# Performance work log

Hardware: AMD Instinct MI355X
Metric: run time of the kernel (lower is better)

Reference implementation:

```python
import jax, jax.numpy as jnp
from jax import lax
import numpy as np

B, DIM, NH, H, W = 4, 256, 8, 32, 32
HEAD_DIM = DIM // NH          # 32
KEY_DIM = HEAD_DIM // 2       # attn_ratio = 0.5 -> 16
QKV_OUT = DIM + 2 * NH * KEY_DIM  # 512
SCALE = KEY_DIM ** -0.5


def setup_inputs() -> dict:
    key = jax.random.key(0)
    ks = jax.random.split(key, 11)
    w = lambda k, shape, s=0.05: jax.random.normal(k, shape, jnp.float32) * s
    return {
        "x": jax.random.normal(ks[0], (B, DIM, H, W), jnp.float32),
        "qkv_w": w(ks[1], (QKV_OUT, DIM)),
        "qkv_b": w(ks[2], (QKV_OUT,)),
        "proj_w": w(ks[3], (DIM, DIM)),
        "proj_b": w(ks[4], (DIM,)),
        "pe_w": w(ks[5], (DIM, 1, 3, 3)),
        "pe_b": w(ks[6], (DIM,)),
        "g1_w": w(ks[7], (DIM // 2, DIM)),
        "g1_b": w(ks[8], (DIM // 2,)),
        "g2_w": w(ks[9], (1, DIM // 2)),
        "g2_b": w(ks[10], (1,)),
    }


def conv1x1(x, w, b):
    # fused Conv2d(1x1, bias=False)+BN -> pointwise matmul + bias
    return jnp.einsum('bchw,oc->bohw', x, w) + b[None, :, None, None]


def reference(x, qkv_w, qkv_b, proj_w, proj_b, pe_w, pe_b, g1_w, g1_b, g2_w, g2_b):
    Bx, C, Hh, Ww = x.shape
    N = Hh * Ww
    qkv = conv1x1(x, qkv_w, qkv_b).reshape(Bx, NH, 2 * KEY_DIM + HEAD_DIM, N)
    q = qkv[:, :, :KEY_DIM]                   # [B, nh, key_dim, N]
    k = qkv[:, :, KEY_DIM:2 * KEY_DIM]        # [B, nh, key_dim, N]
    v = qkv[:, :, 2 * KEY_DIM:]               # [B, nh, head_dim, N]

    # attn = q^T @ k * scale  -> [B, nh, N, N]
    attn = jnp.einsum('bhdn,bhdm->bhnm', q, k) * SCALE

    # learned gate -> scalar dynamic k = floor(N * mean(sigmoid(...)))
    g = jax.nn.sigmoid(conv1x1(jax.nn.relu(conv1x1(x, g1_w, g1_b)), g2_w, g2_b))
    dyn_k = jnp.floor(N * jnp.mean(g)).astype(jnp.int32)

    # rank-based top-k mask (jit-friendly equivalent of topk+scatter):
    # keep entries whose descending rank along the last dim is < dyn_k
    order = jnp.argsort(-attn, axis=-1)       # positions sorted by score desc
    ranks = jnp.argsort(order, axis=-1)       # rank of each position
    attn = jnp.where(ranks < dyn_k, attn, -jnp.inf)
    attn = jax.nn.softmax(attn, axis=-1)

    out = jnp.einsum('bhdn,bhmn->bhdm', v, attn).reshape(Bx, C, Hh, Ww)

    # depthwise 3x3 positional-encoding conv on v reshaped to the image grid
    v_img = v.reshape(Bx, C, Hh, Ww)
    pe = lax.conv_general_dilated(
        v_img, pe_w, window_strides=(1, 1), padding=((1, 1), (1, 1)),
        dimension_numbers=('NCHW', 'OIHW', 'NCHW'), feature_group_count=C,
    ) + pe_b[None, :, None, None]

    return conv1x1(out + pe, proj_w, proj_b)
```

## Files before the change

kernel.cpp:

```cpp
#include <hip/hip_runtime.h>
#include <math.h>

#define NTOK 1024
#define CAP 64

#define LDS_FENCE() asm volatile("s_waitcnt lgkmcnt(0)" ::: "memory")

typedef __bf16 bf16x8 __attribute__((ext_vector_type(8)));
typedef unsigned short u16x8 __attribute__((ext_vector_type(8)));
typedef unsigned short u16x4 __attribute__((ext_vector_type(4)));
typedef float f32x4 __attribute__((ext_vector_type(4)));

__device__ __forceinline__ unsigned short f2bf(float f) {
  unsigned int u = __float_as_uint(f);
  return (unsigned short)((u + 0x7fffu + ((u >> 16) & 1u)) >> 16);
}


template<int OC, int OCB, int P, bool RELU, bool VCAST>
__device__ __forceinline__ void conv_body(const float* __restrict__ in,
    const float* __restrict__ w, const float* __restrict__ bias, float* __restrict__ out,
    unsigned short* __restrict__ vbf, int bid, int tid) {
  constexpr int PB = NTOK / (256 * P);
  const int pb = bid % PB; bid /= PB;
  const int ocb = bid % (OC / OCB); const int b = bid / (OC / OCB);
  const int p0 = pb * 256 * P + tid * P;
  const float* inb = in + (size_t)b * 256 * NTOK + p0;
  const float* wrow = w + (size_t)ocb * OCB * 256;

  float acc[OCB][P];
  #pragma unroll
  for (int j = 0; j < OCB; j++)
    #pragma unroll
    for (int i = 0; i < P; i++) acc[j][i] = 0.f;

  #pragma unroll 2
  for (int c0 = 0; c0 < 256; c0 += 4) {
    float4 wl[OCB];
    #pragma unroll
    for (int j = 0; j < OCB; j++) wl[j] = *(const float4*)&wrow[j * 256 + c0];
    #pragma unroll
    for (int cc = 0; cc < 4; cc++) {
      float xr[P];
      if constexpr (P == 4) {
        float4 t = *(const float4*)&inb[(size_t)(c0 + cc) * NTOK];
        xr[0] = t.x; xr[1] = t.y; xr[2] = t.z; xr[3] = t.w;
      } else if constexpr (P == 2) {
        float2 t = *(const float2*)&inb[(size_t)(c0 + cc) * NTOK];
        xr[0] = t.x; xr[1] = t.y;
      } else {
        xr[0] = inb[(size_t)(c0 + cc) * NTOK];
      }
      #pragma unroll
      for (int j = 0; j < OCB; j++) {
        const float wjc = ((const float*)&wl[j])[cc];
        #pragma unroll
        for (int i = 0; i < P; i++) acc[j][i] = fmaf(wjc, xr[i], acc[j][i]);
      }
    }
  }
  #pragma unroll
  for (int j = 0; j < OCB; j++) {
    const int oc = ocb * OCB + j;
    const float bv = bias[oc];
    float r[P];
    #pragma unroll
    for (int i = 0; i < P; i++) {
      float v = acc[j][i] + bv;
      if (RELU) v = fmaxf(v, 0.f);
      r[i] = v;
    }
    float* op = out + ((size_t)b * OC + oc) * NTOK + p0;
    if constexpr (P == 4) *(float4*)op = make_float4(r[0], r[1], r[2], r[3]);
    else if constexpr (P == 2) *(float2*)op = make_float2(r[0], r[1]);
    else *op = r[0];
    if constexpr (VCAST) {
      if ((oc & 63) >= 32) {
        const int c = (oc >> 6) * 32 + (oc & 63) - 32;
        unsigned short* vp = vbf + ((size_t)b * 256 + c) * NTOK + p0;
        #pragma unroll
        for (int i = 0; i < P; i++) vp[i] = f2bf(r[i]);
      }
    }
  }
}

template<int OC, int OCB, int P, bool RELU, bool VCAST>
__global__ __launch_bounds__(256) void conv1x1_kernel(const float* __restrict__ in,
    const float* __restrict__ w, const float* __restrict__ bias, float* __restrict__ out,
    unsigned short* __restrict__ vbf) {
  conv_body<OC, OCB, P, RELU, VCAST>(in, w, bias, out, vbf, blockIdx.x, threadIdx.x);
}

__global__ __launch_bounds__(256) void qkv_gate1_kernel(const float* __restrict__ x,
    const float* __restrict__ qkv_w, const float* __restrict__ qkv_b, float* __restrict__ qkvb,
    unsigned short* __restrict__ vbf,
    const float* __restrict__ g1_w, const float* __restrict__ g1_b, float* __restrict__ gx) {
  const int bid = blockIdx.x;
  if (bid < 512)
    conv_body<512, 8, 2, false, true>(x, qkv_w, qkv_b, qkvb, vbf, bid, threadIdx.x);
  else
    conv_body<128, 8, 2, true, false>(x, g1_w, g1_b, gx, nullptr, bid - 512, threadIdx.x);
}

__global__ __launch_bounds__(256) void gate2_kernel(const float* __restrict__ gx,
    const float* __restrict__ g2_w, const float* __restrict__ g2_b, float* __restrict__ gvals) {
  const int tid = threadIdx.x;
  const int p_l = tid & 15, jg = tid >> 4;
  const int gp = blockIdx.x * 16 + p_l;
  const int b = gp >> 10, p = gp & 1023;
  float s = 0.f;
  const float* gb = gx + ((size_t)b * 128 + jg * 8) * NTOK + p;
  #pragma unroll
  for (int jj = 0; jj < 8; jj++) s = fmaf(g2_w[jg * 8 + jj], gb[(size_t)jj * NTOK], s);
  __shared__ float red[16][17];
  red[jg][p_l] = s;
  __syncthreads();
  if (tid < 16) {
    float a = g2_b[0];
    #pragma unroll
    for (int g = 0; g < 16; g++) a += red[g][tid];
    gvals[blockIdx.x * 16 + tid] = 1.f / (1.f + expf(-a));
  }
}

__global__ void dynk_kernel(const float* __restrict__ gvals, int* __restrict__ dynk) {
  const int t = threadIdx.x;
  double s = 0.0;
  #pragma unroll
  for (int i = 0; i < 16; i++) s += (double)gvals[t + 256 * i];
  __shared__ double red[256];
  red[t] = s;
  __syncthreads();
  for (int st = 128; st > 0; st >>= 1) {
    if (t < st) red[t] += red[t + st];
    __syncthreads();
  }
  if (t == 0) {
    int k = (int)floor(1024.0 * (red[0] / 4096.0));
    *dynk = k < 1 ? 1 : (k > NTOK ? NTOK : k);
  }
}

__global__ __launch_bounds__(512) void attn_kernel(const float* __restrict__ qkv,
    const unsigned short* __restrict__ vbf,
    const int* __restrict__ dynk_p, float* __restrict__ out_attn) {
  const int tid = threadIdx.x;
  const int lane = tid & 63, wv = tid >> 6;
  int bid = blockIdx.x;
  const int mb = bid & 127; bid >>= 7;
  const int h = bid & 7; const int b = bid >> 3;
  const int dyn_k = *dynk_p;

  const float* base = qkv + (size_t)(b * 512 + h * 64) * NTOK;

  __shared__ union RowU { float f[1028]; unsigned short pa[1032]; } rows[8];
  __shared__ float invs[8];
  __shared__ union UU {
    struct {
      int hist[8][64];
      int cnt[8];
      float Bv[8]; int Bn[8];
      struct { float v; int n; } cand[8][CAP];
    } sel;
    float pvred[2][4][8][17];
  } u;

  {
    const float2* k2 = (const float2*)(base + 16 * NTOK);
    const float* qb = base + mb * 8;
    float a0[8], a1[8];
    #pragma unroll
    for (int r = 0; r < 8; r++) { a0[r] = 0.f; a1[r] = 0.f; }
    #pragma unroll
    for (int d = 0; d < 16; d++) {
      float2 kk = k2[d * 512 + tid];
      #pragma unroll
      for (int r = 0; r < 8; r++) {
        const float qv = qb[(size_t)d * NTOK + r];
        a0[r] = fmaf(qv, kk.x, a0[r]);
        a1[r] = fmaf(qv, kk.y, a1[r]);
      }
    }
    #pragma unroll
    for (int r = 0; r < 8; r++)
      ((float2*)rows[r].f)[tid] = make_float2(a0[r] * 0.25f, a1[r] * 0.25f);
  }
  __syncthreads();

  {
    const int r = wv;
    float* smrow = rows[r].f;
    float v[16];
    {
      float4 f0 = ((const float4*)smrow)[lane];
      float4 f1 = ((const float4*)smrow)[64 + lane];
      float4 f2 = ((const float4*)smrow)[128 + lane];
      float4 f3 = ((const float4*)smrow)[192 + lane];
      v[0]=f0.x; v[1]=f0.y; v[2]=f0.z; v[3]=f0.w;
      v[4]=f1.x; v[5]=f1.y; v[6]=f1.z; v[7]=f1.w;
      v[8]=f2.x; v[9]=f2.y; v[10]=f2.z; v[11]=f2.w;
      v[12]=f3.x; v[13]=f3.y; v[14]=f3.z; v[15]=f3.w;
    }
    float mn = v[0], mx = v[0];
    #pragma unroll
    for (int i = 1; i < 16; i++) { mn = fminf(mn, v[i]); mx = fmaxf(mx, v[i]); }
    #pragma unroll
    for (int off = 32; off > 0; off >>= 1) {
      mn = fminf(mn, __shfl_xor(mn, off));
      mx = fmaxf(mx, __shfl_xor(mx, off));
    }

    unsigned int keepmask = 0xFFFFu;
    if (dyn_k < NTOK) {
      float Bv = mx; int Bn = dyn_k - 1;
      const float range = mx - mn;
      const bool fine = (range > 0.f);
      int m = 0;
      if (fine) {
        const float s1 = 64.0f / range;
        u.sel.hist[wv][lane] = 0;
        LDS_FENCE();
        int idx1[16];
        #pragma unroll
        for (int i = 0; i < 16; i++) {
          int ix = (int)((v[i] - mn) * s1);
          ix = ix < 0 ? 0 : (ix > 63 ? 63 : ix);
          idx1[i] = ix;
          atomicAdd(&u.sel.hist[wv][ix], 1);
        }
        LDS_FENCE();
        int cum = u.sel.hist[wv][lane];
        #pragma unroll
        for (int off = 1; off < 64; off <<= 1) {
          int o = __shfl_down(cum, off);
          if (lane + off < 64) cum += o;
        }
        int cumNext = __shfl_down(cum, 1);
        if (lane == 63) cumNext = 0;
        unsigned long long bal = __ballot(cum >= dyn_k && cumNext < dyn_k);
        const int t = (int)__builtin_ctzll(bal);
        const int k2 = dyn_k - __shfl(cumNext, t);
        const float binw = range * (1.0f / 64.0f);
        const float lo = mn + (float)t * binw;
        float s2 = 4096.0f / range;
        if (!(s2 < 3.0e38f)) s2 = 0.f;
        u.sel.hist[wv][lane] = 0;
        LDS_FENCE();
        #pragma unroll
        for (int i = 0; i < 16; i++) {
          if (idx1[i] == t) {
            int ix = (int)((v[i] - lo) * s2);
            ix = ix < 0 ? 0 : (ix > 63 ? 63 : ix);
            atomicAdd(&u.sel.hist[wv][ix], 1);
          }
        }
        LDS_FENCE();
        cum = u.sel.hist[wv][lane];
        #pragma unroll
        for (int off = 1; off < 64; off <<= 1) {
          int o = __shfl_down(cum, off);
          if (lane + off < 64) cum += o;
        }
        cumNext = __shfl_down(cum, 1);
        if (lane == 63) cumNext = 0;
        bal = __ballot(cum >= k2 && cumNext < k2);
        const int t2 = (int)__builtin_ctzll(bal);
        const int k3 = k2 - __shfl(cumNext, t2);
        if (lane == 0) u.sel.cnt[wv] = 0;
        LDS_FENCE();
        #pragma unroll
        for (int i = 0; i < 16; i++) {
          if (idx1[i] == t) {
            int ix = (int)((v[i] - lo) * s2);
            ix = ix < 0 ? 0 : (ix > 63 ? 63 : ix);
            if (ix == t2) {
              int p = atomicAdd(&u.sel.cnt[wv], 1);
              if (p < CAP) { u.sel.cand[wv][p].v = v[i]; u.sel.cand[wv][p].n = (i >> 2) * 256 + lane * 4 + (i & 3); }
            }
          }
        }
        LDS_FENCE();
        m = u.sel.cnt[wv];
        if (m <= CAP) {
          for (int ii = lane; ii < m; ii += 64) {
            float cv = u.sel.cand[wv][ii].v; int cn = u.sel.cand[wv][ii].n;
            int rk = 0;
            for (int j = 0; j < m; j++) {
              float ov = u.sel.cand[wv][j].v; int on = u.sel.cand[wv][j].n;
              rk += ((ov > cv) || (ov == cv && on < cn)) ? 1 : 0;
            }
            if (rk == k3 - 1) { u.sel.Bv[wv] = cv; u.sel.Bn[wv] = cn; }
          }
          LDS_FENCE();
          Bv = u.sel.Bv[wv]; Bn = u.sel.Bn[wv];
        }
      }
      if (fine && m > CAP) {
        keepmask = 0u;
        #pragma unroll
        for (int i = 0; i < 16; i++) {
          const int n_i = (i >> 2) * 256 + lane * 4 + (i & 3);
          const float vi = v[i];
          int rk = 0;
          for (int j = 0; j < NTOK; j++) {
            float ov = smrow[j];
            rk += ((ov > vi) || (ov == vi && j < n_i)) ? 1 : 0;
          }
          if (rk < dyn_k) keepmask |= (1u << i);
        }
      } else {
        keepmask = 0u;
        #pragma unroll
        for (int i = 0; i < 16; i++) {
          const int n_i = (i >> 2) * 256 + lane * 4 + (i & 3);
          if ((v[i] > Bv) || (v[i] == Bv && n_i <= Bn)) keepmask |= (1u << i);
        }
      }
    }
    float e[16]; float s = 0.f;
    #pragma unroll
    for (int i = 0; i < 16; i++) {
      e[i] = ((keepmask >> i) & 1u) ? __expf(v[i] - mx) : 0.f;
      s += e[i];
    }
    #pragma unroll
    for (int off = 32; off > 0; off >>= 1) s += __shfl_xor(s, off);
    if (lane == 0) invs[r] = 1.f / s;
    #pragma unroll
    for (int j = 0; j < 4; j++) {
      u16x4 w4 = { f2bf(e[4*j]), f2bf(e[4*j+1]), f2bf(e[4*j+2]), f2bf(e[4*j+3]) };
      *(u16x4*)&rows[r].pa[j * 256 + lane * 4] = w4;
    }
  }
  __syncthreads();

  {
    const int g = lane >> 4;
    const int m16 = lane & 15;
    const int ksl = wv & 3, dt = wv >> 2;
    const unsigned short* vrow = vbf + ((size_t)(b * 256 + h * 32 + dt * 16 + m16)) * NTOK;
    const unsigned short* parow = rows[lane & 7].pa;
    f32x4 acc = {0.f, 0.f, 0.f, 0.f};
    const int nb = ksl * 256;
    #pragma unroll
    for (int ks = 0; ks < 8; ks++) {
      const int n0 = nb + ks * 32 + g * 8;
      bf16x8 a  = __builtin_bit_cast(bf16x8, *(const u16x8*)&parow[n0]);
      bf16x8 b0 = __builtin_bit_cast(bf16x8, *(const u16x8*)&vrow[n0]);
      acc = __builtin_amdgcn_mfma_f32_16x16x32_bf16(a, b0, acc, 0, 0, 0);
    }
    if (g < 2) {
      #pragma unroll
      for (int q = 0; q < 4; q++)
        u.pvred[dt][ksl][g * 4 + q][m16] = acc[q];
    }
  }
  __syncthreads();
  if (tid < 256) {
    const int r2 = tid & 7, d2 = tid >> 3;
    const int dt = d2 >> 4, m16 = d2 & 15;
    float s = u.pvred[dt][0][r2][m16] + u.pvred[dt][1][r2][m16]
            + u.pvred[dt][2][r2][m16] + u.pvred[dt][3][r2][m16];
    s *= invs[r2];
    out_attn[(size_t)(b * 256 + h * 32 + d2) * NTOK + mb * 8 + r2] = s;
  }
}

__global__ __launch_bounds__(256) void pe_kernel(const float* __restrict__ qkv,
    const float* __restrict__ oattn, const float* __restrict__ pe_w,
    const float* __restrict__ pe_b, float* __restrict__ tmp) {
  int bid = blockIdx.x;
  const int c = bid & 255; const int b = bid >> 8;
  const int oc = ((c >> 5) * 64) + 32 + (c & 31);
  const float* vimg = qkv + (size_t)(b * 512 + oc) * NTOK;
  float wloc[9];
  #pragma unroll
  for (int i = 0; i < 9; i++) wloc[i] = pe_w[c * 9 + i];
  const float bv = pe_b[c];
  const int t = threadIdx.x;
  const int p0 = t * 4;
  const int y = p0 >> 5, x0 = p0 & 31;
  float win[3][6];
  #pragma unroll
  for (int dy = -1; dy <= 1; dy++) {
    const int yy = y + dy;
    float* wr = win[dy + 1];
    if (yy < 0 || yy > 31) {
      #pragma unroll
      for (int i = 0; i < 6; i++) wr[i] = 0.f;
    } else {
      const float* vr = vimg + yy * 32;
      wr[0] = (x0 > 0) ? vr[x0 - 1] : 0.f;
      const float4 mid = *(const float4*)&vr[x0];
      wr[1] = mid.x; wr[2] = mid.y; wr[3] = mid.z; wr[4] = mid.w;
      wr[5] = (x0 < 28) ? vr[x0 + 4] : 0.f;
    }
  }
  const float4 oa = *(const float4*)(oattn + (size_t)(b * 256 + c) * NTOK + p0);
  float r[4];
  #pragma unroll
  for (int i = 0; i < 4; i++) {
    float s = bv;
    #pragma unroll
    for (int dy = 0; dy < 3; dy++) {
      s = fmaf(wloc[dy * 3 + 0], win[dy][i], s);
      s = fmaf(wloc[dy * 3 + 1], win[dy][i + 1], s);
      s = fmaf(wloc[dy * 3 + 2], win[dy][i + 2], s);
    }
    r[i] = s;
  }
  float4 o = make_float4(r[0] + oa.x, r[1] + oa.y, r[2] + oa.z, r[3] + oa.w);
  *(float4*)(tmp + (size_t)(b * 256 + c) * NTOK + p0) = o;
}

extern "C" void kernel_launch(void* const* d_in, const int* in_sizes, int n_in,
                              void* d_out, int out_size, void* d_ws, size_t ws_size,
                              hipStream_t stream) {
  const float* x      = (const float*)d_in[0];
  const float* qkv_w  = (const float*)d_in[1];
  const float* qkv_b  = (const float*)d_in[2];
  const float* proj_w = (const float*)d_in[3];
  const float* proj_b = (const float*)d_in[4];
  const float* pe_w   = (const float*)d_in[5];
  const float* pe_b   = (const float*)d_in[6];
  const float* g1_w   = (const float*)d_in[7];
  const float* g1_b   = (const float*)d_in[8];
  const float* g2_w   = (const float*)d_in[9];
  const float* g2_b   = (const float*)d_in[10];
  float* out = (float*)d_out;

  char* ws = (char*)d_ws;
  float*  qkvb  = (float*)(ws);
  float*  oattn = (float*)(ws + (8u << 20));
  float*  tmp   = (float*)(ws + (12u << 20));
  unsigned short* vbf = (unsigned short*)(ws + (12u << 20));
  float*  gx    = (float*)(ws + (16u << 20));
  float*  gvals = (float*)(ws + (18u << 20));
  int*    dynk  = (int*)(ws + (18u << 20) + (64u << 10));

  qkv_gate1_kernel<<<640, 256, 0, stream>>>(x, qkv_w, qkv_b, qkvb, vbf, g1_w, g1_b, gx);
  gate2_kernel<<<256, 256, 0, stream>>>(gx, g2_w, g2_b, gvals);
  dynk_kernel<<<1, 256, 0, stream>>>(gvals, dynk);
  attn_kernel<<<4096, 512, 0, stream>>>(qkvb, vbf, dynk, oattn);
  pe_kernel<<<1024, 256, 0, stream>>>(qkvb, oattn, pe_w, pe_b, tmp);
  conv1x1_kernel<256, 8, 1, false, false><<<512, 256, 0, stream>>>(tmp, proj_w, proj_b, out, nullptr);
}
```

Before: 141.5 us.

## Compute attention scores with split-bf16 MFMA using prepacked K layout

The QKV projection now also writes K in a prepacked bf16 hi/lo split layout tiled for MFMA. The attention kernel's q·k score computation, previously a scalar fp32 FMA loop reading K from the fp32 buffer, now uses 16x16x32 bf16 MFMA with hi/lo splits to approximate fp32 accuracy. The aim is to cut score-computation ALU work and K load bandwidth. The cost is extra scattered 2-byte stores in the conv kernel and some precision loss, since the q lo-part product with K is only partly compensated.

After: 158.4 us. +11.9%, slower.

```diff
diff --git a/kernel.cpp b/kernel.cpp
--- a/kernel.cpp
+++ b/kernel.cpp
@@ -15,12 +15,15 @@
   unsigned int u = __float_as_uint(f);
   return (unsigned short)((u + 0x7fffu + ((u >> 16) & 1u)) >> 16);
 }
+__device__ __forceinline__ float bf2f(unsigned short h) {
+  return __uint_as_float((unsigned int)h << 16);
+}
 
 
 template<int OC, int OCB, int P, bool RELU, bool VCAST>
 __device__ __forceinline__ void conv_body(const float* __restrict__ in,
     const float* __restrict__ w, const float* __restrict__ bias, float* __restrict__ out,
-    unsigned short* __restrict__ vbf, int bid, int tid) {
+    unsigned short* __restrict__ vbf, unsigned short* __restrict__ kpack, int bid, int tid) {
   constexpr int PB = NTOK / (256 * P);
   const int pb = bid % PB; bid /= PB;
   const int ocb = bid % (OC / OCB); const int b = bid / (OC / OCB);
@@ -75,11 +78,25 @@
     else if constexpr (P == 2) *(float2*)op = make_float2(r[0], r[1]);
     else *op = r[0];
     if constexpr (VCAST) {
-      if ((oc & 63) >= 32) {
-        const int c = (oc >> 6) * 32 + (oc & 63) - 32;
+      const int c63 = oc & 63;
+      if (c63 >= 32) {
+        const int c = (oc >> 6) * 32 + c63 - 32;
         unsigned short* vp = vbf + ((size_t)b * 256 + c) * NTOK + p0;
         #pragma unroll
         for (int i = 0; i < P; i++) vp[i] = f2bf(r[i]);
+      } else if (c63 >= 16) {
+        const int h = oc >> 6, d = c63 - 16;
+        const int gh = d >> 3, jj = d & 7;
+        unsigned short* kb = kpack + (size_t)(b * 8 + h) * 32768;
+        #pragma unroll
+        for (int i = 0; i < P; i++) {
+          const int n = p0 + i;
+          const int t = n >> 4, n16 = n & 15;
+          const unsigned short hv = f2bf(r[i]);
+          const unsigned short lv = f2bf(r[i] - bf2f(hv));
+          kb[((t * 4 + gh) * 16 + n16) * 8 + jj]     = hv;
+          kb[((t * 4 + gh + 2) * 16 + n16) * 8 + jj] = lv;
+        }
       }
     }
   }
@@ -89,18 +106,18 @@
 __global__ __launch_bounds__(256) void conv1x1_kernel(const float* __restrict__ in,
     const float* __restrict__ w, const float* __restrict__ bias, float* __restrict__ out,
     unsigned short* __restrict__ vbf) {
-  conv_body<OC, OCB, P, RELU, VCAST>(in, w, bias, out, vbf, blockIdx.x, threadIdx.x);
+  conv_body<OC, OCB, P, RELU, VCAST>(in, w, bias, out, vbf, nullptr, blockIdx.x, threadIdx.x);
 }
 
 __global__ __launch_bounds__(256) void qkv_gate1_kernel(const float* __restrict__ x,
     const float* __restrict__ qkv_w, const float* __restrict__ qkv_b, float* __restrict__ qkvb,
-    unsigned short* __restrict__ vbf,
+    unsigned short* __restrict__ vbf, unsigned short* __restrict__ kpack,
     const float* __restrict__ g1_w, const float* __restrict__ g1_b, float* __restrict__ gx) {
   const int bid = blockIdx.x;
   if (bid < 512)
-    conv_body<512, 8, 2, false, true>(x, qkv_w, qkv_b, qkvb, vbf, bid, threadIdx.x);
+    conv_body<512, 8, 2, false, true>(x, qkv_w, qkv_b, qkvb, vbf, kpack, bid, threadIdx.x);
   else
-    conv_body<128, 8, 2, true, false>(x, g1_w, g1_b, gx, nullptr, bid - 512, threadIdx.x);
+    conv_body<128, 8, 2, true, false>(x, g1_w, g1_b, gx, nullptr, nullptr, bid - 512, threadIdx.x);
 }
 
 __global__ __launch_bounds__(256) void gate2_kernel(const float* __restrict__ gx,
@@ -143,7 +160,7 @@
 }
 
 __global__ __launch_bounds__(512) void attn_kernel(const float* __restrict__ qkv,
-    const unsigned short* __restrict__ vbf,
+    const unsigned short* __restrict__ vbf, const unsigned short* __restrict__ kpack,
     const int* __restrict__ dynk_p, float* __restrict__ out_attn) {
   const int tid = threadIdx.x;
   const int lane = tid & 63, wv = tid >> 6;
@@ -167,24 +184,31 @@
   } u;
 
   {
-    const float2* k2 = (const float2*)(base + 16 * NTOK);
-    const float* qb = base + mb * 8;
-    float a0[8], a1[8];
-    #pragma unroll
-    for (int r = 0; r < 8; r++) { a0[r] = 0.f; a1[r] = 0.f; }
-    #pragma unroll
-    for (int d = 0; d < 16; d++) {
-      float2 kk = k2[d * 512 + tid];
+    const unsigned short* kb = kpack + (size_t)(b * 8 + h) * 32768;
+    const int g = lane >> 4, m16 = lane & 15;
+    u16x8 b1u = {0, 0, 0, 0, 0, 0, 0, 0}, b2u = {0, 0, 0, 0, 0, 0, 0, 0};
+    if (m16 < 8) {
+      const float* qcol = base + (size_t)((g & 1) * 8) * NTOK + mb * 8 + m16;
       #pragma unroll
-      for (int r = 0; r < 8; r++) {
-        const float qv = qb[(size_t)d * NTOK + r];
-        a0[r] = fmaf(qv, kk.x, a0[r]);
-        a1[r] = fmaf(qv, kk.y, a1[r]);
-      }
-    }
-    #pragma unroll
-    for (int r = 0; r < 8; r++)
-      ((float2*)rows[r].f)[tid] = make_float2(a0[r] * 0.25f, a1[r] * 0.25f);
+      for (int jj = 0; jj < 8; jj++) {
+        const float qv = qcol[(size_t)jj * NTOK] * 0.25f;
+        const unsigned short hv = f2bf(qv);
+        b1u[jj] = hv;
+        b2u[jj] = f2bf(qv - bf2f(hv));
+      }
+    }
+    bf16x8 B1 = __builtin_bit_cast(bf16x8, b1u);
+    bf16x8 B2 = __builtin_bit_cast(bf16x8, b2u);
+    #pragma unroll
+    for (int i = 0; i < 8; i++) {
+      const int t = wv * 8 + i;
+      bf16x8 A = __builtin_bit_cast(bf16x8, *(const u16x8*)&kb[((t * 4 + g) * 16 + m16) * 8]);
+      f32x4 acc = {0.f, 0.f, 0.f, 0.f};
+      acc = __builtin_amdgcn_mfma_f32_16x16x32_bf16(A, B1, acc, 0, 0, 0);
+      acc = __builtin_amdgcn_mfma_f32_16x16x32_bf16(A, B2, acc, 0, 0, 0);
+      if (m16 < 8)
+        *(f32x4*)&rows[m16].f[t * 16 + g * 4] = acc;
+    }
   }
   __syncthreads();
 
@@ -434,15 +458,16 @@
   float*  qkvb  = (float*)(ws);
   float*  oattn = (float*)(ws + (8u << 20));
   float*  tmp   = (float*)(ws + (12u << 20));
-  unsigned short* vbf = (unsigned short*)(ws + (12u << 20));
+  unsigned short* vbf   = (unsigned short*)(ws + (12u << 20));
+  unsigned short* kpack = (unsigned short*)(ws + (14u << 20));
   float*  gx    = (float*)(ws + (16u << 20));
   float*  gvals = (float*)(ws + (18u << 20));
   int*    dynk  = (int*)(ws + (18u << 20) + (64u << 10));
 
-  qkv_gate1_kernel<<<640, 256, 0, stream>>>(x, qkv_w, qkv_b, qkvb, vbf, g1_w, g1_b, gx);
+  qkv_gate1_kernel<<<640, 256, 0, stream>>>(x, qkv_w, qkv_b, qkvb, vbf, kpack, g1_w, g1_b, gx);
   gate2_kernel<<<256, 256, 0, stream>>>(gx, g2_w, g2_b, gvals);
   dynk_kernel<<<1, 256, 0, stream>>>(gvals, dynk);
-  attn_kernel<<<4096, 512, 0, stream>>>(qkvb, vbf, dynk, oattn);
+  attn_kernel<<<4096, 512, 0, stream>>>(qkvb, vbf, kpack, dynk, oattn);
   pe_kernel<<<1024, 256, 0, stream>>>(qkvb, oattn, pe_w, pe_b, tmp);
   conv1x1_kernel<256, 8, 1, false, false><<<512, 256, 0, stream>>>(tmp, proj_w, proj_b, out, nullptr);
 }
```
